# Performance work log

Hardware: AMD Instinct MI355X
Metric: run time of the kernel (lower is better)

The kernel has to match this reference:

```python
import jax, jax.numpy as jnp
import numpy as np

# ---- configuration (mirrors cfg used by the torch module) ----
H = W = 64          # cfg.KEYPOINT.HEATMAP_SIZE
C = 256             # cfg.KEYPOINT.NFEATS
N = 2               # batch (number of view pairs)
S = 32              # cfg.EPIPOLAR.SAMPLESIZE
DS = 4              # cfg.BACKBONE.DOWNSAMPLE
EPS = 1e-3          # self.epsilon


def pix2coord(v):
    # feature-map pixel -> original-image coordinate
    return v * DS + DS / 2.0 - 0.5


def _camera_pair():
    # realistic stereo pair: image is 256x256 (64x64 heatmap * downsample 4)
    K = np.array([[300.0, 0.0, 127.5], [0.0, 300.0, 127.5], [0.0, 0.0, 1.0]])
    P1 = K @ np.hstack([np.eye(3), np.zeros((3, 1))])
    ang = np.deg2rad(15.0)
    R = np.array([[np.cos(ang), 0, np.sin(ang)], [0, 1, 0], [-np.sin(ang), 0, np.cos(ang)]])
    t = np.array([[-0.5], [0.0], [0.1]])
    P2 = K @ np.hstack([R, t])
    return P1.astype(np.float32), P2.astype(np.float32)


def setup_inputs() -> dict:
    key = jax.random.key(0)
    k1, k2 = jax.random.split(key)
    feat1 = jax.random.normal(k1, (N, C, H, W), dtype=jnp.float32)
    feat2 = jax.random.normal(k2, (N, C, H, W), dtype=jnp.float32)
    P1np, P2np = _camera_pair()
    P1 = jnp.asarray(np.stack([P1np] * N))
    P2 = jnp.asarray(np.stack([P2np] * N))
    return {"feat1": feat1, "feat2": feat2, "P1": P1, "P2": P2}


def _fundamental(P1, P2):
    # F = [e2]_x P2 P1^+ ; camera center = null vector of P1
    P1inv = jnp.linalg.pinv(P1)          # 4x3
    _, _, Vt = jnp.linalg.svd(P1)
    Cc = Vt[-1]                          # homogeneous camera center, (4,)
    e2 = P2 @ Cc                         # epipole in view 2, (3,)
    z = jnp.zeros(())
    skew = jnp.stack([jnp.stack([z, -e2[2], e2[1]]),
                      jnp.stack([e2[2], z, -e2[0]]),
                      jnp.stack([-e2[1], e2[0], z])])
    return skew @ (P2 @ P1inv)


def _sample_locs(P1, P2):
    """Epipolar-line sample locations, [S, N, H, W, 2] normalized to [-1,1]."""
    xs = pix2coord(jnp.arange(W, dtype=jnp.float32))
    ys = pix2coord(jnp.arange(H, dtype=jnp.float32))
    xmin, xmax = xs[0], xs[-1]
    ymin, ymax = ys[0], ys[-1]
    gy, gx = jnp.meshgrid(ys, xs, indexing='ij')
    grid = jnp.stack([gx.ravel(), gy.ravel(), jnp.ones(H * W, jnp.float32)])

    F = jax.vmap(_fundamental)(P1, P2)
    lines = jnp.einsum('nij,jp->nip', F, grid)
    a, b, c = lines[:, 0], lines[:, 1], lines[:, 2]
    a_s = jnp.where(jnp.abs(a) < EPS, EPS, a)
    b_s = jnp.where(jnp.abs(b) < EPS, EPS, b)
    # intersections of a*x + b*y + c = 0 with the 4 image borders
    y_at_xmin = -(c + a * xmin) / b_s
    y_at_xmax = -(c + a * xmax) / b_s
    x_at_ymin = -(c + b * ymin) / a_s
    x_at_ymax = -(c + b * ymax) / a_s
    cx = jnp.stack([jnp.full_like(a, xmin), jnp.full_like(a, xmax), x_at_ymin, x_at_ymax], -1)  # N,HW,4
    cy = jnp.stack([y_at_xmin, y_at_xmax, jnp.full_like(a, ymin), jnp.full_like(a, ymax)], -1)
    tol = 1e-2
    valid = (cx >= xmin - tol) & (cx <= xmax + tol) & (cy >= ymin - tol) & (cy <= ymax + tol)
    # invalid -> far out of range (equivalent of self.outrange_tensor);
    # such sample locs fall outside [-1,1] and contribute zeros in grid_sample
    cx = jnp.where(valid, cx, xmin - 10000.0)
    cy = jnp.where(valid, cy, ymin - 10000.0)
    order = jnp.argsort(jnp.logical_not(valid), axis=-1)  # stable: valid candidates first
    pick = order[..., :2]                                 # N,HW,2
    px = jnp.take_along_axis(cx, pick, axis=-1)
    py = jnp.take_along_axis(cy, pick, axis=-1)
    # normalize original-image coords to [-1,1] over the feature grid extent
    nx = (px - xmin) / (xmax - xmin) * 2.0 - 1.0
    ny = (py - ymin) / (ymax - ymin) * 2.0 - 1.0
    start = jnp.stack([nx[..., 0], ny[..., 0]], -1)       # N,HW,2
    end = jnp.stack([nx[..., 1], ny[..., 1]], -1)
    steps = jnp.linspace(0.0, 1.0, S).reshape(S, 1, 1, 1)
    locs = start[None] + steps * (end - start)[None]      # S,N,HW,2
    return locs.reshape(S, N, H, W, 2)


def _grid_sample(img, grid):
    """Bilinear sampling with zeros padding. img [C,H,W], grid [S,H,W,2] -> [S,C,H,W]."""
    gx, gy = grid[..., 0], grid[..., 1]
    x = (gx + 1.0) * 0.5 * (W - 1)
    y = (gy + 1.0) * 0.5 * (H - 1)
    x0 = jnp.floor(x)
    y0 = jnp.floor(y)
    wx = x - x0
    wy = y - y0
    x0i = x0.astype(jnp.int32)
    y0i = y0.astype(jnp.int32)

    def gather(yi, xi, w):
        inb = (yi >= 0) & (yi <= H - 1) & (xi >= 0) & (xi <= W - 1)
        yc = jnp.clip(yi, 0, H - 1)
        xc = jnp.clip(xi, 0, W - 1)
        vals = img[:, yc, xc]                  # C,S,H,W
        return vals * (w * inb)[None]

    out = (gather(y0i, x0i, (1 - wy) * (1 - wx))
           + gather(y0i, x0i + 1, (1 - wy) * wx)
           + gather(y0i + 1, x0i, wy * (1 - wx))
           + gather(y0i + 1, x0i + 1, wy * wx))
    return out.transpose(1, 0, 2, 3)           # S,C,H,W


def reference(feat1, feat2, P1, P2):
    # geometry (torch.no_grad in original)
    locs = jax.lax.stop_gradient(_sample_locs(P1, P2))   # S,N,H,W,2
    locs_n = jnp.transpose(locs, (1, 0, 2, 3, 4))        # N,S,H,W,2
    sampled = jax.vmap(_grid_sample)(feat2, locs_n)      # N,S,C,H,W
    # dot-product similarity + softmax attention over the epipolar samples ('avg')
    sim = jax.nn.softmax(jnp.einsum('nchw,nschw->nshw', feat1, sampled), axis=1)
    out = jnp.einsum('nshw,nschw->nchw', sim, sampled)   # N,C,H,W
    return out
```

## Files before the change

kernel.cpp:

```cpp
#include <hip/hip_runtime.h>
#include <math.h>

#define H 64
#define W 64
#define C 256
#define NB 2
#define SS 32
#define HW (H*W)

typedef __attribute__((ext_vector_type(2))) _Float16 half2v;
typedef __attribute__((ext_vector_type(2))) __fp16   fp16x2;

__device__ __forceinline__ half2v pk2(float a) {
  return __builtin_bit_cast(half2v, __builtin_amdgcn_cvt_pkrtz(a, a));
}

__device__ __forceinline__ float fdot2(half2v a, half2v b, float c) {
#if __has_builtin(__builtin_amdgcn_fdot2)
  return __builtin_amdgcn_fdot2(__builtin_bit_cast(fp16x2, a),
                                __builtin_bit_cast(fp16x2, b), c, false);
#else
  c = fmaf((float)a.x, (float)b.x, c);
  c = fmaf((float)a.y, (float)b.y, c);
  return c;
#endif
}

__device__ void fmat_compute(const float* __restrict__ P1f,
                             const float* __restrict__ P2f,
                             double* __restrict__ Fout, int n) {
  double p1[3][4], p2[3][4];
  for (int i = 0; i < 3; ++i)
    for (int j = 0; j < 4; ++j) {
      p1[i][j] = (double)P1f[n * 12 + i * 4 + j];
      p2[i][j] = (double)P2f[n * 12 + i * 4 + j];
    }
  double A[3][3];
  for (int i = 0; i < 3; ++i)
    for (int j = 0; j < 3; ++j) {
      double s = 0;
      for (int k = 0; k < 4; ++k) s += p1[i][k] * p1[j][k];
      A[i][j] = s;
    }
  double det = A[0][0] * (A[1][1] * A[2][2] - A[1][2] * A[2][1])
             - A[0][1] * (A[1][0] * A[2][2] - A[1][2] * A[2][0])
             + A[0][2] * (A[1][0] * A[2][1] - A[1][1] * A[2][0]);
  double id = 1.0 / det;
  double Ai[3][3];
  Ai[0][0] = (A[1][1] * A[2][2] - A[1][2] * A[2][1]) * id;
  Ai[0][1] = (A[0][2] * A[2][1] - A[0][1] * A[2][2]) * id;
  Ai[0][2] = (A[0][1] * A[1][2] - A[0][2] * A[1][1]) * id;
  Ai[1][0] = (A[1][2] * A[2][0] - A[1][0] * A[2][2]) * id;
  Ai[1][1] = (A[0][0] * A[2][2] - A[0][2] * A[2][0]) * id;
  Ai[1][2] = (A[0][2] * A[1][0] - A[0][0] * A[1][2]) * id;
  Ai[2][0] = (A[1][0] * A[2][1] - A[1][1] * A[2][0]) * id;
  Ai[2][1] = (A[0][1] * A[2][0] - A[0][0] * A[2][1]) * id;
  Ai[2][2] = (A[0][0] * A[1][1] - A[0][1] * A[1][0]) * id;
  double Pi[4][3];
  for (int i = 0; i < 4; ++i)
    for (int j = 0; j < 3; ++j) {
      double s = 0;
      for (int k = 0; k < 3; ++k) s += p1[k][i] * Ai[k][j];
      Pi[i][j] = s;
    }
  double M[3][3];
  for (int i = 0; i < 3; ++i)
    for (int j = 0; j < 3; ++j) {
      double s = 0;
      for (int k = 0; k < 4; ++k) s += p2[i][k] * Pi[k][j];
      M[i][j] = s;
    }
  double nv[4];
  {
    auto det3 = [&](int ca, int cb, int cc) {
      return p1[0][ca] * (p1[1][cb] * p1[2][cc] - p1[1][cc] * p1[2][cb])
           - p1[0][cb] * (p1[1][ca] * p1[2][cc] - p1[1][cc] * p1[2][ca])
           + p1[0][cc] * (p1[1][ca] * p1[2][cb] - p1[1][cb] * p1[2][ca]);
    };
    nv[0] =  det3(1, 2, 3);
    nv[1] = -det3(0, 2, 3);
    nv[2] =  det3(0, 1, 3);
    nv[3] = -det3(0, 1, 2);
  }
  double nn = sqrt(nv[0]*nv[0] + nv[1]*nv[1] + nv[2]*nv[2] + nv[3]*nv[3]);
  for (int i = 0; i < 4; ++i) nv[i] /= nn;
  double e2[3];
  for (int i = 0; i < 3; ++i) {
    double s = 0;
    for (int j = 0; j < 4; ++j) s += p2[i][j] * nv[j];
    e2[i] = s;
  }
  for (int j = 0; j < 3; ++j) {
    Fout[n * 9 + 0 * 3 + j] = -e2[2] * M[1][j] + e2[1] * M[2][j];
    Fout[n * 9 + 1 * 3 + j] =  e2[2] * M[0][j] - e2[0] * M[2][j];
    Fout[n * 9 + 2 * 3 + j] = -e2[1] * M[0][j] + e2[0] * M[1][j];
  }
}

__global__ __launch_bounds__(256) void prep_kernel(
    const float* __restrict__ feat2,
    const float* __restrict__ P1f, const float* __restrict__ P2f,
    _Float16* __restrict__ f2t, double* __restrict__ Fd) {
  __shared__ float tile[32][33];
  const int n  = blockIdx.z;
  const int p0 = blockIdx.x * 32;
  const int c0 = blockIdx.y * 32;
  const int tx = threadIdx.x, ty = threadIdx.y;
  const float* src = feat2 + (size_t)n * (C * HW);
#pragma unroll
  for (int j = 0; j < 4; ++j) {
    int cc = c0 + ty + j * 8;
    tile[ty + j * 8][tx] = src[(size_t)cc * HW + p0 + tx];
  }
  __syncthreads();
  {
    const int tid = ty * 32 + tx;
    const int pp = tid >> 3;
    const int cp = tid & 7;
    _Float16* dst = f2t + (size_t)n * (HW * C) + (size_t)(p0 + pp) * C + c0;
#pragma unroll
    for (int jj = 0; jj < 2; ++jj) {
      const int cc = (cp + jj * 8) * 2;
      half2v h2;
      h2.x = (_Float16)tile[cc][pp];
      h2.y = (_Float16)tile[cc + 1][pp];
      *(half2v*)(dst + cc) = h2;
    }
  }
  if (n == 0 && blockIdx.x == 0 && blockIdx.y == 0) {
    int t = ty * 32 + tx;
    if (t < NB) fmat_compute(P1f, P2f, Fd, t);
  }
}

__device__ __forceinline__ float groupsum32(float v) {
  v += __int_as_float(__builtin_amdgcn_update_dpp(
         0, __float_as_int(v), 0xB1, 0xF, 0xF, true));
  v += __int_as_float(__builtin_amdgcn_update_dpp(
         0, __float_as_int(v), 0x4E, 0xF, 0xF, true));
  v += __int_as_float(__builtin_amdgcn_update_dpp(
         0, __float_as_int(v), 0x124, 0xF, 0xF, true));
  v += __int_as_float(__builtin_amdgcn_update_dpp(
         0, __float_as_int(v), 0x128, 0xF, 0xF, true));
#if __has_builtin(__builtin_amdgcn_permlane16_swap)
  {
    auto pr = __builtin_amdgcn_permlane16_swap(
        __float_as_int(v), __float_as_int(v), false, false);
    v = __int_as_float(pr[0]) + __int_as_float(pr[1]);
  }
#else
  v += __int_as_float(__builtin_amdgcn_ds_swizzle(
         __float_as_int(v), 0x401F));
#endif
  return v;
}

__global__ __launch_bounds__(256) void epi_main(
    const float* __restrict__ feat1, const _Float16* __restrict__ f2t,
    const double* __restrict__ Fd, float* __restrict__ out) {
  const int tid  = threadIdx.x;
  const int lane = tid & 63;
  const int wv   = tid >> 6;
  const int grp  = lane >> 5;
  const int cl   = lane & 31;
  const int bid  = blockIdx.x;
  const int r    = bid & 7;
  const int k    = bid >> 3;
  const int n    = r >> 2;
  const int sub  = r & 3;
  const int p    = (sub * 128 + k) * 8 + wv * 2 + grp;
  const int h = p >> 6, w = p & (W - 1);
  const int cb = cl * 8;

  half2v f1h[4];
  {
    const float* f1b = feat1 + ((size_t)n * C + cb) * HW + p;
#pragma unroll
    for (int i = 0; i < 4; ++i) {
      const float lo = f1b[(size_t)(2 * i) * HW];
      const float hi = f1b[(size_t)(2 * i + 1) * HW];
      f1h[i] = __builtin_bit_cast(half2v, __builtin_amdgcn_cvt_pkrtz(lo, hi));
    }
  }

  const double* Fdp = Fd + n * 9;
  const float F0 = (float)Fdp[0], F1 = (float)Fdp[1], F2 = (float)Fdp[2];
  const float F3 = (float)Fdp[3], F4 = (float)Fdp[4], F5 = (float)Fdp[5];
  const float F6 = (float)Fdp[6], F7 = (float)Fdp[7], F8 = (float)Fdp[8];
  const float X = w * 4.0f + 1.5f;
  const float Y = h * 4.0f + 1.5f;
  const float a = F0 * X + F1 * Y + F2;
  const float b = F3 * X + F4 * Y + F5;
  const float c = F6 * X + F7 * Y + F8;
  const float a_s = (fabsf(a) < 1e-3f) ? 1e-3f : a;
  const float b_s = (fabsf(b) < 1e-3f) ? 1e-3f : b;
  const float xmin = 1.5f, xmax = 253.5f, ymin = 1.5f, ymax = 253.5f, tol = 0.01f;
  float cx[4], cy[4];
  cx[0] = xmin;  cy[0] = -(c + a * xmin) / b_s;
  cx[1] = xmax;  cy[1] = -(c + a * xmax) / b_s;
  cx[2] = -(c + b * ymin) / a_s;  cy[2] = ymin;
  cx[3] = -(c + b * ymax) / a_s;  cy[3] = ymax;
  bool valid[4];
#pragma unroll
  for (int i = 0; i < 4; ++i)
    valid[i] = (cx[i] >= xmin - tol) && (cx[i] <= xmax + tol) &&
               (cy[i] >= ymin - tol) && (cy[i] <= ymax + tol);
#pragma unroll
  for (int i = 0; i < 4; ++i)
    if (!valid[i]) { cx[i] = xmin - 10000.0f; cy[i] = ymin - 10000.0f; }
  int pk0 = -1, pk1 = -1;
#pragma unroll
  for (int i = 0; i < 4; ++i)
    if (valid[i]) { if (pk0 < 0) pk0 = i; else if (pk1 < 0) pk1 = i; }
#pragma unroll
  for (int i = 0; i < 4; ++i)
    if (!valid[i]) { if (pk0 < 0) pk0 = i; else if (pk1 < 0) pk1 = i; }
  const float x0p = (cx[pk0] - 1.5f) * 0.25f;
  const float y0p = (cy[pk0] - 1.5f) * 0.25f;
  const float pdx = (cx[pk1] - 1.5f) * 0.25f - x0p;
  const float pdy = (cy[pk1] - 1.5f) * 0.25f - y0p;
  const float dx = pdx * (1.0f / 31.0f);
  const float dy = pdy * (1.0f / 31.0f);

  const _Float16* f2b = f2t + (size_t)n * HW * C + cb;

  float m = -1e30f, l = 0.f;
  half2v acc2[4];
#pragma unroll
  for (int i = 0; i < 4; ++i) acc2[i] = (half2v)(_Float16)0;

  auto fetch = [&](float x, float y, uint4& A, uint4& B, uint4& Cc, uint4& D,
                   half2v& wa, half2v& wb, half2v& wc, half2v& wd) {
    const float xf = floorf(x), yf = floorf(y);
    const float wx = x - xf, wy = y - yf;
    const int x0 = (int)xf, y0 = (int)yf;
    const bool bx0 = ((unsigned)x0 < W), bx1 = ((unsigned)(x0 + 1) < W);
    const bool by0 = ((unsigned)y0 < H), by1 = ((unsigned)(y0 + 1) < H);
    const int xc0 = min(max(x0, 0), W - 1);
    const int xc1 = min(max(x0 + 1, 0), W - 1);
    const int yc0 = min(max(y0, 0), H - 1);
    const int yc1 = min(max(y0 + 1, 0), H - 1);
    const float ux0 = bx0 ? (1.f - wx) : 0.f;
    const float ux1 = bx1 ? wx : 0.f;
    const float vy0 = by0 ? (1.f - wy) : 0.f;
    const float vy1 = by1 ? wy : 0.f;
    wa = pk2(vy0 * ux0);
    wb = pk2(vy0 * ux1);
    wc = pk2(vy1 * ux0);
    wd = pk2(vy1 * ux1);
    const int r0 = yc0 * W, r1 = yc1 * W;
    A  = *(const uint4*)(f2b + (r0 + xc0) * C);
    B  = *(const uint4*)(f2b + (r0 + xc1) * C);
    Cc = *(const uint4*)(f2b + (r1 + xc0) * C);
    D  = *(const uint4*)(f2b + (r1 + xc1) * C);
  };

  auto bilin = [&](const uint4& A, const uint4& B, const uint4& Cc,
                   const uint4& D, half2v wa, half2v wb, half2v wc, half2v wd,
                   half2v q[4], float& part) {
    const uint* ap = (const uint*)&A;
    const uint* bp = (const uint*)&B;
    const uint* cp = (const uint*)&Cc;
    const uint* dp = (const uint*)&D;
    part = 0.f;
#pragma unroll
    for (int j = 0; j < 4; ++j) {
      half2v qa = __builtin_bit_cast(half2v, ap[j]) * wa;
      qa += __builtin_bit_cast(half2v, bp[j]) * wb;
      qa += __builtin_bit_cast(half2v, cp[j]) * wc;
      qa += __builtin_bit_cast(half2v, dp[j]) * wd;
      q[j] = qa;
      part = fdot2(qa, f1h[j], part);
    }
  };

  float xs = x0p, ys = y0p;
#pragma unroll
  for (int s = 0; s < SS; s += 2) {
    uint4 A0, B0, C0, D0, A1, B1, C1, D1;
    half2v wa0, wb0, wc0, wd0, wa1, wb1, wc1, wd1;
    fetch(xs,      ys,      A0, B0, C0, D0, wa0, wb0, wc0, wd0);
    fetch(xs + dx, ys + dy, A1, B1, C1, D1, wa1, wb1, wc1, wd1);
    xs += 2.f * dx;
    ys += 2.f * dy;

    half2v q0[4], q1[4];
    float p0, p1;
    bilin(A0, B0, C0, D0, wa0, wb0, wc0, wd0, q0, p0);
    bilin(A1, B1, C1, D1, wa1, wb1, wc1, wd1, q1, p1);
    p0 = groupsum32(p0);
    p1 = groupsum32(p1);

    const float mx = fmaxf(p0, p1);
    if (__any(mx > m + 4.f)) {
      const float mn = fmaxf(m, mx);
      const float sc = __expf(m - mn);
      l *= sc;
      const half2v sch = pk2(sc);
#pragma unroll
      for (int i = 0; i < 4; ++i) acc2[i] *= sch;
      m = mn;
    }
    const float e0 = __expf(p0 - m);
    const float e1 = __expf(p1 - m);
    l += e0 + e1;
    const half2v eh0 = pk2(e0);
    const half2v eh1 = pk2(e1);
#pragma unroll
    for (int i = 0; i < 4; ++i) {
      acc2[i] += eh0 * q0[i];
      acc2[i] += eh1 * q1[i];
    }
  }

  const float inv = 1.0f / l;
  float* ob = out + (size_t)n * C * HW + (size_t)cb * HW + p;
#pragma unroll
  for (int i = 0; i < 4; ++i) {
    ob[(size_t)(2 * i) * HW]     = (float)acc2[i].x * inv;
    ob[(size_t)(2 * i + 1) * HW] = (float)acc2[i].y * inv;
  }
}

extern "C" void kernel_launch(void* const* d_in, const int* in_sizes, int n_in,
                              void* d_out, int out_size, void* d_ws, size_t ws_size,
                              hipStream_t stream) {
  const float* feat1 = (const float*)d_in[0];
  const float* feat2 = (const float*)d_in[1];
  const float* P1 = (const float*)d_in[2];
  const float* P2 = (const float*)d_in[3];
  float* out = (float*)d_out;

  char* ws = (char*)d_ws;
  _Float16* f2t = (_Float16*)ws;
  double*   Fd  = (double*)(ws + (5u << 20));

  prep_kernel<<<dim3(HW / 32, C / 32, NB), dim3(32, 8), 0, stream>>>(
      feat2, P1, P2, f2t, Fd);
  epi_main<<<NB * HW / 8, 256, 0, stream>>>(feat1, f2t, Fd, out);
}
```

Baseline: 39.26 us.

## Assign one pixel per wavefront, splitting bilinear corner pairs across half-waves

Each wavefront now handles one pixel instead of two. The two 32-lane halves fetch adjacent-x corner pixels in one contiguous 1KB load per row, so each lane issues two loads per sample instead of four. Weights are remapped so that clamped border cases still select the correct corners. The per-sample reduction now spans the full 64 lanes, and the fp16 accumulators are combined across halves before only half the lanes write the output. This cuts per-lane load and FMA work but doubles the block count and adds a cross-half shuffle reduction.

```diff
diff --git a/kernel.cpp b/kernel.cpp
--- a/kernel.cpp
+++ b/kernel.cpp
@@ -133,7 +133,7 @@
   }
 }
 
-__device__ __forceinline__ float groupsum32(float v) {
+__device__ __forceinline__ float wavesum64(float v) {
   v += __int_as_float(__builtin_amdgcn_update_dpp(
          0, __float_as_int(v), 0xB1, 0xF, 0xF, true));
   v += __int_as_float(__builtin_amdgcn_update_dpp(
@@ -142,16 +142,8 @@
          0, __float_as_int(v), 0x124, 0xF, 0xF, true));
   v += __int_as_float(__builtin_amdgcn_update_dpp(
          0, __float_as_int(v), 0x128, 0xF, 0xF, true));
-#if __has_builtin(__builtin_amdgcn_permlane16_swap)
-  {
-    auto pr = __builtin_amdgcn_permlane16_swap(
-        __float_as_int(v), __float_as_int(v), false, false);
-    v = __int_as_float(pr[0]) + __int_as_float(pr[1]);
-  }
-#else
-  v += __int_as_float(__builtin_amdgcn_ds_swizzle(
-         __float_as_int(v), 0x401F));
-#endif
+  v += __shfl_xor(v, 16);
+  v += __shfl_xor(v, 32);
   return v;
 }
 
@@ -161,14 +153,14 @@
   const int tid  = threadIdx.x;
   const int lane = tid & 63;
   const int wv   = tid >> 6;
-  const int grp  = lane >> 5;
+  const bool halfB = lane >= 32;
   const int cl   = lane & 31;
   const int bid  = blockIdx.x;
   const int r    = bid & 7;
   const int k    = bid >> 3;
   const int n    = r >> 2;
   const int sub  = r & 3;
-  const int p    = (sub * 128 + k) * 8 + wv * 2 + grp;
+  const int p    = sub * 1024 + k * 4 + wv;
   const int h = p >> 6, w = p & (W - 1);
   const int cb = cl * 8;
 
@@ -222,74 +214,67 @@
   const float dx = pdx * (1.0f / 31.0f);
   const float dy = pdy * (1.0f / 31.0f);
 
-  const _Float16* f2b = f2t + (size_t)n * HW * C + cb;
+  const _Float16* f2i = f2t + (size_t)n * HW * C + lane * 8;
 
   float m = -1e30f, l = 0.f;
   half2v acc2[4];
 #pragma unroll
   for (int i = 0; i < 4; ++i) acc2[i] = (half2v)(_Float16)0;
 
-  auto fetch = [&](float x, float y, uint4& A, uint4& B, uint4& Cc, uint4& D,
-                   half2v& wa, half2v& wb, half2v& wc, half2v& wd) {
+  auto fetch = [&](float x, float y, uint4& L0, uint4& L1,
+                   float& w0f, float& w1f) {
     const float xf = floorf(x), yf = floorf(y);
     const float wx = x - xf, wy = y - yf;
     const int x0 = (int)xf, y0 = (int)yf;
     const bool bx0 = ((unsigned)x0 < W), bx1 = ((unsigned)(x0 + 1) < W);
     const bool by0 = ((unsigned)y0 < H), by1 = ((unsigned)(y0 + 1) < H);
-    const int xc0 = min(max(x0, 0), W - 1);
-    const int xc1 = min(max(x0 + 1, 0), W - 1);
-    const int yc0 = min(max(y0, 0), H - 1);
-    const int yc1 = min(max(y0 + 1, 0), H - 1);
+    const int bc = min(max(x0, 0), W - 1);
+    const int br = min(max(y0, 0), H - 1);
     const float ux0 = bx0 ? (1.f - wx) : 0.f;
     const float ux1 = bx1 ? wx : 0.f;
     const float vy0 = by0 ? (1.f - wy) : 0.f;
     const float vy1 = by1 ? wy : 0.f;
-    wa = pk2(vy0 * ux0);
-    wb = pk2(vy0 * ux1);
-    wc = pk2(vy1 * ux0);
-    wd = pk2(vy1 * ux1);
-    const int r0 = yc0 * W, r1 = yc1 * W;
-    A  = *(const uint4*)(f2b + (r0 + xc0) * C);
-    B  = *(const uint4*)(f2b + (r0 + xc1) * C);
-    Cc = *(const uint4*)(f2b + (r1 + xc0) * C);
-    D  = *(const uint4*)(f2b + (r1 + xc1) * C);
+    const float w00 = vy0 * ux0, w01 = vy0 * ux1;
+    const float w10 = vy1 * ux0, w11 = vy1 * ux1;
+    const bool yneg = (y0 < 0);
+    const float ra0 = yneg ? w10 : w00, ra1 = yneg ? w11 : w01;
+    const float rb0 = yneg ? 0.f : w10, rb1 = yneg ? 0.f : w11;
+    const bool xneg = (x0 < 0);
+    const float sa = xneg ? ra1 : ra0, sb = xneg ? 0.f : ra1;
+    const float ta = xneg ? rb1 : rb0, tb = xneg ? 0.f : rb1;
+    w0f = halfB ? sb : sa;
+    w1f = halfB ? tb : ta;
+    const int br2 = min(br + 1, H - 1);
+    L0 = *(const uint4*)(f2i + (size_t)(br  * W + bc) * C);
+    L1 = *(const uint4*)(f2i + (size_t)(br2 * W + bc) * C);
   };
 
-  auto bilin = [&](const uint4& A, const uint4& B, const uint4& Cc,
-                   const uint4& D, half2v wa, half2v wb, half2v wc, half2v wd,
-                   half2v q[4], float& part) {
-    const uint* ap = (const uint*)&A;
-    const uint* bp = (const uint*)&B;
-    const uint* cp = (const uint*)&Cc;
-    const uint* dp = (const uint*)&D;
-    part = 0.f;
+  auto dots = [&](const uint4& L0, const uint4& L1, float& d0, float& d1) {
+    const uint* p0w = (const uint*)&L0;
+    const uint* p1w = (const uint*)&L1;
+    d0 = 0.f; d1 = 0.f;
 #pragma unroll
     for (int j = 0; j < 4; ++j) {
-      half2v qa = __builtin_bit_cast(half2v, ap[j]) * wa;
-      qa += __builtin_bit_cast(half2v, bp[j]) * wb;
-      qa += __builtin_bit_cast(half2v, cp[j]) * wc;
-      qa += __builtin_bit_cast(half2v, dp[j]) * wd;
-      q[j] = qa;
-      part = fdot2(qa, f1h[j], part);
+      d0 = fdot2(__builtin_bit_cast(half2v, p0w[j]), f1h[j], d0);
+      d1 = fdot2(__builtin_bit_cast(half2v, p1w[j]), f1h[j], d1);
     }
   };
 
   float xs = x0p, ys = y0p;
 #pragma unroll
   for (int s = 0; s < SS; s += 2) {
-    uint4 A0, B0, C0, D0, A1, B1, C1, D1;
-    half2v wa0, wb0, wc0, wd0, wa1, wb1, wc1, wd1;
-    fetch(xs,      ys,      A0, B0, C0, D0, wa0, wb0, wc0, wd0);
-    fetch(xs + dx, ys + dy, A1, B1, C1, D1, wa1, wb1, wc1, wd1);
+    uint4 A0, A1, B0, B1;
+    float wa0, wa1, wb0, wb1;
+    fetch(xs,      ys,      A0, A1, wa0, wa1);
+    fetch(xs + dx, ys + dy, B0, B1, wb0, wb1);
     xs += 2.f * dx;
     ys += 2.f * dy;
 
-    half2v q0[4], q1[4];
-    float p0, p1;
-    bilin(A0, B0, C0, D0, wa0, wb0, wc0, wd0, q0, p0);
-    bilin(A1, B1, C1, D1, wa1, wb1, wc1, wd1, q1, p1);
-    p0 = groupsum32(p0);
-    p1 = groupsum32(p1);
+    float da0, da1, db0, db1;
+    dots(A0, A1, da0, da1);
+    dots(B0, B1, db0, db1);
+    float p0 = wavesum64(fmaf(wa0, da0, wa1 * da1));
+    float p1 = wavesum64(fmaf(wb0, db0, wb1 * db1));
 
     const float mx = fmaxf(p0, p1);
     if (__any(mx > m + 4.f)) {
@@ -304,21 +289,38 @@
     const float e0 = __expf(p0 - m);
     const float e1 = __expf(p1 - m);
     l += e0 + e1;
-    const half2v eh0 = pk2(e0);
-    const half2v eh1 = pk2(e1);
+    const half2v eh0 = pk2(e0), eh1 = pk2(e1);
+    const half2v wA0 = pk2(wa0), wA1 = pk2(wa1);
+    const half2v wB0 = pk2(wb0), wB1 = pk2(wb1);
+    const uint* a0w = (const uint*)&A0;
+    const uint* a1w = (const uint*)&A1;
+    const uint* b0w = (const uint*)&B0;
+    const uint* b1w = (const uint*)&B1;
 #pragma unroll
     for (int i = 0; i < 4; ++i) {
-      acc2[i] += eh0 * q0[i];
-      acc2[i] += eh1 * q1[i];
-    }
+      half2v q0 = __builtin_bit_cast(half2v, a0w[i]) * wA0 +
+                  __builtin_bit_cast(half2v, a1w[i]) * wA1;
+      half2v q1 = __builtin_bit_cast(half2v, b0w[i]) * wB0 +
+                  __builtin_bit_cast(half2v, b1w[i]) * wB1;
+      acc2[i] += eh0 * q0;
+      acc2[i] += eh1 * q1;
+    }
+  }
+
+#pragma unroll
+  for (int i = 0; i < 4; ++i) {
+    const int sw = __shfl_xor(__builtin_bit_cast(int, acc2[i]), 32);
+    acc2[i] = acc2[i] + __builtin_bit_cast(half2v, sw);
   }
 
   const float inv = 1.0f / l;
-  float* ob = out + (size_t)n * C * HW + (size_t)cb * HW + p;
-#pragma unroll
-  for (int i = 0; i < 4; ++i) {
-    ob[(size_t)(2 * i) * HW]     = (float)acc2[i].x * inv;
-    ob[(size_t)(2 * i + 1) * HW] = (float)acc2[i].y * inv;
+  if (!halfB) {
+    float* ob = out + (size_t)n * C * HW + (size_t)cb * HW + p;
+#pragma unroll
+    for (int i = 0; i < 4; ++i) {
+      ob[(size_t)(2 * i) * HW]     = (float)acc2[i].x * inv;
+      ob[(size_t)(2 * i + 1) * HW] = (float)acc2[i].y * inv;
+    }
   }
 }
 
@@ -337,5 +339,5 @@
 
   prep_kernel<<<dim3(HW / 32, C / 32, NB), dim3(32, 8), 0, stream>>>(
       feat2, P1, P2, f2t, Fd);
-  epi_main<<<NB * HW / 8, 256, 0, stream>>>(feat1, f2t, Fd, out);
-}
+  epi_main<<<NB * HW / 4, 256, 0, stream>>>(feat1, f2t, Fd, out);
+}
```

Measured after the change: 54.91 us. 39.9% more time.

## Split epipolar samples across two waves and merge softmax partials via LDS

Applied to the files above, without the earlier changes.

Each pixel pair is now handled by two waves, each processing half of the 32 epipolar samples. That shortens the serial fetch, softmax and accumulate chain per wave and doubles the wave count. The partial max, sum and fp16 accumulators are combined through shared memory with an online-softmax rescale before writing the output. The cost is duplicated feat1 loads, a block barrier, LDS traffic, twice as many smaller blocks, and an extra fp16 rounding step in the merge.

```diff
diff --git a/kernel.cpp b/kernel.cpp
--- a/kernel.cpp
+++ b/kernel.cpp
@@ -155,12 +155,12 @@
   return v;
 }
 
-__global__ __launch_bounds__(256) void epi_main(
+__global__ __launch_bounds__(128) void epi_main(
     const float* __restrict__ feat1, const _Float16* __restrict__ f2t,
     const double* __restrict__ Fd, float* __restrict__ out) {
   const int tid  = threadIdx.x;
   const int lane = tid & 63;
-  const int wv   = tid >> 6;
+  const int sh   = tid >> 6;
   const int grp  = lane >> 5;
   const int cl   = lane & 31;
   const int bid  = blockIdx.x;
@@ -168,7 +168,7 @@
   const int k    = bid >> 3;
   const int n    = r >> 2;
   const int sub  = r & 3;
-  const int p    = (sub * 128 + k) * 8 + wv * 2 + grp;
+  const int p    = sub * 1024 + k * 2 + grp;
   const int h = p >> 6, w = p & (W - 1);
   const int cb = cl * 8;
 
@@ -274,9 +274,10 @@
     }
   };
 
-  float xs = x0p, ys = y0p;
-#pragma unroll
-  for (int s = 0; s < SS; s += 2) {
+  float xs = fmaf((float)(sh * 16), dx, x0p);
+  float ys = fmaf((float)(sh * 16), dy, y0p);
+#pragma unroll
+  for (int s = 0; s < SS / 2; s += 2) {
     uint4 A0, B0, C0, D0, A1, B1, C1, D1;
     half2v wa0, wb0, wc0, wd0, wa1, wb1, wc1, wd1;
     fetch(xs,      ys,      A0, B0, C0, D0, wa0, wb0, wc0, wd0);
@@ -313,12 +314,31 @@
     }
   }
 
-  const float inv = 1.0f / l;
-  float* ob = out + (size_t)n * C * HW + (size_t)cb * HW + p;
-#pragma unroll
-  for (int i = 0; i < 4; ++i) {
-    ob[(size_t)(2 * i) * HW]     = (float)acc2[i].x * inv;
-    ob[(size_t)(2 * i + 1) * HW] = (float)acc2[i].y * inv;
+  __shared__ float lsm[64][8];
+  if (sh) {
+#pragma unroll
+    for (int i = 0; i < 4; ++i)
+      lsm[lane][i] = __int_as_float(__builtin_bit_cast(int, acc2[i]));
+    lsm[lane][4] = m;
+    lsm[lane][5] = l;
+  }
+  __syncthreads();
+  if (!sh) {
+    const float mo = lsm[lane][4], lo = lsm[lane][5];
+    const float mf = fmaxf(m, mo);
+    const float e0 = __expf(m - mf), e1 = __expf(mo - mf);
+    const float L = l * e0 + lo * e1;
+    const float inv = 1.0f / L;
+    const half2v eh0 = pk2(e0), eh1 = pk2(e1);
+    float* ob = out + (size_t)n * C * HW + (size_t)cb * HW + p;
+#pragma unroll
+    for (int i = 0; i < 4; ++i) {
+      const half2v bo = __builtin_bit_cast(half2v,
+                          __float_as_int(lsm[lane][i]));
+      const half2v merged = acc2[i] * eh0 + bo * eh1;
+      ob[(size_t)(2 * i) * HW]     = (float)merged.x * inv;
+      ob[(size_t)(2 * i + 1) * HW] = (float)merged.y * inv;
+    }
   }
 }
 
@@ -337,5 +357,5 @@
 
   prep_kernel<<<dim3(HW / 32, C / 32, NB), dim3(32, 8), 0, stream>>>(
       feat2, P1, P2, f2t, Fd);
-  epi_main<<<NB * HW / 8, 256, 0, stream>>>(feat1, f2t, Fd, out);
-}
+  epi_main<<<NB * HW / 2, 128, 0, stream>>>(feat1, f2t, Fd, out);
+}
```

After: 40.84 us. 1.04x slower.
